# Optimization experiments

Hardware: AMD Instinct MI355X
Metric: run time of the kernel (lower is better)

## Reference

```python
import jax, jax.numpy as jnp
import numpy as np

ALPHA = 0.2  # LeakyReLU negative slope
NEG_INF = -9e15


def _gat_layer(Wh, adj, a, concat):
    """One GraphAttentionLayer given pre-projected Wh [B,N,F].
    Algebraic split of the concat attention: e[b,i,j] = lrelu(Wh[i]@a1 + Wh[j]@a2),
    identical math to matmul(cat(Wh_i, Wh_j), a)."""
    F_ = Wh.shape[-1]
    f1 = Wh @ a[:F_, 0]   # [B,N]
    f2 = Wh @ a[F_:, 0]   # [B,N]
    e = jax.nn.leaky_relu(f1[:, :, None] + f2[:, None, :], negative_slope=ALPHA)  # [B,N,N]
    e = jnp.where(adj > 0, e, NEG_INF)
    att = jax.nn.softmax(e, axis=-1)            # dropout omitted (eval mode)
    h_prime = jnp.einsum('bij,bjf->bif', att, Wh)
    return jax.nn.elu(h_prime) if concat else h_prime


def setup_inputs() -> dict:
    key = jax.random.key(0)
    ks = jax.random.split(key, 9)
    B, N, Fin, H, nH, Fout = 4, 2048, 512, 128, 4, 256
    x = jax.random.normal(ks[0], (B, N, Fin), dtype=jnp.float32)
    adj = jax.random.randint(ks[1], (B, N, N), 0, 2, dtype=jnp.int32)
    mask = jnp.ones((B, N), dtype=jnp.float32)
    s = 0.05
    W_heads = jax.random.normal(ks[2], (nH, Fin, H), dtype=jnp.float32) * s
    a_heads = jax.random.normal(ks[3], (nH, 2 * H, 1), dtype=jnp.float32) * s
    W_out = jax.random.normal(ks[4], (nH * H, Fout), dtype=jnp.float32) * s
    a_out = jax.random.normal(ks[5], (2 * Fout, 1), dtype=jnp.float32) * s
    W_pool = jax.random.normal(ks[6], (Fout, Fout), dtype=jnp.float32) * s
    b_pool = jax.random.normal(ks[7], (Fout,), dtype=jnp.float32) * s
    return {"x": x, "adj": adj, "mask": mask, "W_heads": W_heads, "a_heads": a_heads,
            "W_out": W_out, "a_out": a_out, "W_pool": W_pool, "b_pool": b_pool}


def reference(x, adj, mask, W_heads, a_heads, W_out, a_out, W_pool, b_pool):
    # multi-head GAT layer, heads concatenated (dropout = identity in eval)
    heads = [_gat_layer(x @ W_heads[h], adj, a_heads[h], concat=True)
             for h in range(W_heads.shape[0])]
    xcat = jnp.concatenate(heads, axis=-1)                 # [B,N,nH*H]
    x_out = _gat_layer(xcat @ W_out, adj, a_out, concat=False)  # [B,N,Fout]
    x_out = x_out * mask[:, :, None]
    pooled = x_out.sum(axis=1) / (mask.sum(axis=1, keepdims=True) + 1e-10)
    graph_embedding = jax.nn.relu(pooled @ W_pool + b_pool)
    return graph_embedding, x_out
```

## Files before the change

kernel.cpp:

```cpp
#include <hip/hip_runtime.h>

typedef unsigned short u16;
typedef __attribute__((ext_vector_type(8))) short s8v;
typedef __attribute__((ext_vector_type(8))) unsigned short us8;
typedef __attribute__((ext_vector_type(4))) float f4v;
typedef __attribute__((ext_vector_type(2))) float fp2;

#define L2E 1.4426950408889634f

typedef __attribute__((address_space(1))) void gvoid_t;
typedef __attribute__((address_space(3))) void lvoid_t;

__device__ __forceinline__ u16 f2bf(float f) {
  unsigned u = __builtin_bit_cast(unsigned, f);
  return (u16)((u + 0x7FFFu + ((u >> 16) & 1u)) >> 16);
}
__device__ __forceinline__ float bf2f(u16 h) {
  return __builtin_bit_cast(float, ((unsigned)h) << 16);
}
__device__ __forceinline__ f4v mfma16(s8v a, s8v b, f4v c) {
  return __builtin_amdgcn_mfma_f32_16x16x32_bf16(a, b, c, 0, 0, 0);
}
__device__ __forceinline__ float exp2fast(float x) {
#if __has_builtin(__builtin_amdgcn_exp2f)
  return __builtin_amdgcn_exp2f(x);
#else
  return exp2f(x);
#endif
}
__device__ __forceinline__ void stage16(const u16* g, u16* lds_arr, int slot) {
#if __has_builtin(__builtin_amdgcn_global_load_lds)
  __builtin_amdgcn_global_load_lds((gvoid_t*)(g),
      (lvoid_t*)(lds_arr + (size_t)(slot & ~63) * 8), 16, 0, 0);
#else
  *(us8*)(lds_arr + (size_t)slot * 8) = *(const us8*)g;
#endif
}

__global__ __launch_bounds__(256) void prep_all(const float* __restrict__ x,
                                                u16* __restrict__ xb,
                                                const float* __restrict__ Wh,
                                                u16* __restrict__ Wta,
                                                const float* __restrict__ Wo,
                                                u16* __restrict__ Wto) {
  int bid = blockIdx.x;
  if (bid < 2048) {
    int i = (bid * 256 + threadIdx.x) * 8;
    float4 v0 = *(const float4*)(x + i);
    float4 v1 = *(const float4*)(x + i + 4);
    us8 o;
    o[0] = f2bf(v0.x); o[1] = f2bf(v0.y); o[2] = f2bf(v0.z); o[3] = f2bf(v0.w);
    o[4] = f2bf(v1.x); o[5] = f2bf(v1.y); o[6] = f2bf(v1.z); o[7] = f2bf(v1.w);
    *(us8*)(xb + i) = o;
  } else if (bid < 3072) {
    int idx = (bid - 2048) * 256 + threadIdx.x;
    int h = idx >> 16, k = (idx >> 7) & 511, f = idx & 127;
    Wta[(size_t)(h * 128 + f) * 512 + k] = f2bf(Wh[idx]);
  } else {
    int idx = (bid - 3072) * 256 + threadIdx.x;
    int k = idx >> 8, c = idx & 255;
    Wto[(size_t)c * 512 + k] = f2bf(Wo[idx]);
  }
}

__global__ __launch_bounds__(256) void prep_adj(const int* __restrict__ adj,
                                                unsigned* __restrict__ adjw) {
  int chunk = blockIdx.x * 4 + (threadIdx.x >> 6);
  int l = threadIdx.x & 63;
  int v = adj[(size_t)chunk * 64 + l];
  unsigned long long m = __ballot(v != 0);
  if (l == 0) {
    ((uint2*)adjw)[chunk] = make_uint2((unsigned)m, (unsigned)(m >> 32));
  }
}

__global__ __launch_bounds__(256) void gemm_bf16(const u16* __restrict__ A,
                                                 const u16* __restrict__ Bt,
                                                 u16* __restrict__ Ct, int CO) {
  const int K = 512, N = 2048;
  int m0 = blockIdx.x * 64;
  int n0 = blockIdx.y * 64;
  int t = threadIdx.x;
  int w = t >> 6, l = t & 63, lr = l & 15, lq = l >> 4;
  int wr = w >> 1, wc = w & 1;
  __shared__ u16 As[2][64 * 32];
  __shared__ u16 Bs[2][64 * 32];
  f4v zero4 = {0.f, 0.f, 0.f, 0.f};
  f4v acc[2][2];
#pragma unroll
  for (int i = 0; i < 2; ++i)
#pragma unroll
    for (int j = 0; j < 2; ++j) acc[i][j] = zero4;

  auto stage = [&](int buf, int kt) {
    int k0 = kt * 32;
    int row = t >> 2, ch = t & 3;
    int q = (ch ^ ((row >> 1) & 3)) * 8;
    stage16(A + (size_t)(m0 + row) * K + k0 + q, As[buf], t);
    stage16(Bt + (size_t)(n0 + row) * K + k0 + q, Bs[buf], t);
  };
  stage(0, 0);
  int swz = (lq ^ ((lr >> 1) & 3)) * 8;
  for (int kt = 0; kt < 16; ++kt) {
    __syncthreads();
    if (kt < 15) stage((kt + 1) & 1, kt + 1);
    const u16* as = As[kt & 1];
    const u16* bs = Bs[kt & 1];
    s8v af[2], bfr[2];
#pragma unroll
    for (int rf = 0; rf < 2; ++rf)
      af[rf] = *(const s8v*)&as[(wr * 32 + rf * 16 + lr) * 32 + swz];
#pragma unroll
    for (int nf = 0; nf < 2; ++nf)
      bfr[nf] = *(const s8v*)&bs[(wc * 32 + nf * 16 + lr) * 32 + swz];
#pragma unroll
    for (int rf = 0; rf < 2; ++rf)
#pragma unroll
      for (int nf = 0; nf < 2; ++nf)
        acc[rf][nf] = mfma16(af[rf], bfr[nf], acc[rf][nf]);
  }
  int bidx = m0 >> 11;
  int nr0 = m0 & 2047;
#pragma unroll
  for (int rf = 0; rf < 2; ++rf) {
#pragma unroll
    for (int nf = 0; nf < 2; ++nf) {
      int col = n0 + wc * 32 + nf * 16 + lr;
      int nr = nr0 + wr * 32 + rf * 16 + lq * 4;
      f4v a = acc[rf][nf];
      ushort4 v = make_ushort4(f2bf(a[0]), f2bf(a[1]), f2bf(a[2]), f2bf(a[3]));
      *(ushort4*)&Ct[((size_t)bidx * CO + col) * N + nr] = v;
    }
  }
}

__global__ __launch_bounds__(256) void fkern(const u16* __restrict__ Wht,
                                             const float* __restrict__ a,
                                             float* __restrict__ f1L,
                                             float* __restrict__ f2L, int COLS,
                                             int F) {
  const int N = 2048;
  int h = blockIdx.z, b = blockIdx.y;
  int nl = threadIdx.x & 63, fc = threadIdx.x >> 6;
  int n = blockIdx.x * 64 + nl;
  int F4 = F >> 2;
  const u16* colp = Wht + ((size_t)(b * COLS + h * F + fc * F4)) * N + n;
  const float* ah = a + h * 2 * F + fc * F4;
  float a1 = 0.f, a2 = 0.f;
  for (int c = 0; c < F4; ++c) {
    float v = bf2f(colp[(size_t)c * N]);
    a1 = fmaf(v, ah[c], a1);
    a2 = fmaf(v, ah[F + c], a2);
  }
  __shared__ float r1[4][64], r2[4][64];
  r1[fc][nl] = a1;
  r2[fc][nl] = a2;
  __syncthreads();
  if (fc == 0) {
    float s1 = r1[0][nl] + r1[1][nl] + r1[2][nl] + r1[3][nl];
    float s2 = r2[0][nl] + r2[1][nl] + r2[2][nl] + r2[3][nl];
    f1L[(size_t)(h * 4 + b) * N + n] = s1 * L2E;
    f2L[(size_t)(h * 4 + b) * N + n] = s2 * L2E;
  }
}

__global__ __launch_bounds__(256) void fmax_kern(const float* __restrict__ f2L,
                                                 float* __restrict__ f2m) {
  int row = blockIdx.x;
  const float* p = f2L + (size_t)row * 2048;
  int t = threadIdx.x;
  float v = -__builtin_inff();
  for (int k = 0; k < 8; ++k) v = fmaxf(v, p[t + k * 256]);
#pragma unroll
  for (int d = 1; d < 64; d <<= 1) v = fmaxf(v, __shfl_xor(v, d));
  __shared__ float wm[4];
  if ((t & 63) == 0) wm[t >> 6] = v;
  __syncthreads();
  if (t == 0) f2m[row] = fmaxf(fmaxf(wm[0], wm[1]), fmaxf(wm[2], wm[3]));
}

template <int CT, int WR, bool ELU>
__global__ __launch_bounds__(256, 2) void attn_kernel(
    const u16* __restrict__ Wht, const float* __restrict__ f1L,
    const float* __restrict__ f2L, const float* __restrict__ f2max,
    const unsigned* __restrict__ adjw, const float* __restrict__ mask,
    void* __restrict__ outp, float* __restrict__ pool) {
  const int N = 2048;
  constexpr int WC = 4 / WR;
  constexpr int NF = 8 / WC;
  constexpr int NCH = CT / 128;
  constexpr int ROWS = WR * 16;
  constexpr int NT = 2048 / ROWS;
  constexpr int FHD = (CT == 512) ? 1 : 0;
  int kb = blockIdx.x;
  int x = kb & 7, g = kb >> 3;
  int p = x + 8 * (g / NT);
  int it = g % NT;
  int b = p / NCH, ch = p % NCH;
  int i0 = it * ROWS, col0 = ch * 128;
  int fh = FHD ? ch : 0;
  int t = threadIdx.x;
  int w = t >> 6, l = t & 63, lr = l & 15, lq = l >> 4;
  int wc = w & (WC - 1), wrs = w / WC;

  __shared__ u16 Vs[2][128 * 64];
  __shared__ unsigned adjs[ROWS * 65];
  __shared__ float f2s[2048];

  const float* f1p = f1L + (size_t)(fh * 4 + b) * N + i0;
  const float* f2p = f2L + (size_t)(fh * 4 + b) * N;
  float f2m = f2max[fh * 4 + b];
  float f1v = f1p[wrs * 16 + lr];
  float su = f1v + f2m;
  float M = fmaxf(su, 0.2f * su);
  float c1 = f1v - M;
  float c2 = 0.2f * f1v - M;
  fp2 c1p = {c1, c1}, c2p = {c2, c2}, k2p = {0.2f, 0.2f};
  const u16* vbase = Wht + (size_t)(b * CT + col0) * 2048;

  for (int i = t; i < ROWS * 64; i += 256) {
    int row = i >> 6, wd = i & 63;
    adjs[row * 65 + wd] = adjw[(size_t)(b * N + i0 + row) * 64 + wd];
  }
  for (int i = t; i < 2048; i += 256) f2s[i] = f2p[i];

  auto stage = [&](int buf, int kt) {
    int k0 = kt * 64;
#pragma unroll
    for (int j2 = 0; j2 < 4; ++j2) {
      int s = j2 * 256 + t;
      int c = s >> 3, q = s & 7;
      stage16(vbase + (size_t)c * 2048 + k0 + (q ^ (c & 7)) * 8, Vs[buf], s);
    }
  };
  stage(0, 0);

  f4v zero4 = {0.f, 0.f, 0.f, 0.f};
  f4v acc[NF], accs = zero4;
#pragma unroll
  for (int j = 0; j < NF; ++j) acc[j] = zero4;
  s8v ones;
#pragma unroll
  for (int i = 0; i < 8; ++i) ones[i] = (short)0x3F80;

  for (int kt = 0; kt < 32; ++kt) {
    __syncthreads();
    if (kt < 31) stage((kt + 1) & 1, kt + 1);
    const u16* vs = Vs[kt & 1];
#pragma unroll
    for (int kk = 0; kk < 2; ++kk) {
      int jt = kt * 2 + kk;
      s8v vf[NF];
#pragma unroll
      for (int nf = 0; nf < NF; ++nf) {
        int c = wc * 64 + nf * 16 + lr;
        int chn = (kk * 4 + lq) ^ (lr & 7);
        vf[nf] = *(const s8v*)&vs[c * 64 + chn * 8];
      }
      float4 fa = *(const float4*)&f2s[jt * 32 + lq * 8];
      float4 fb = *(const float4*)&f2s[jt * 32 + lq * 8 + 4];
      float f2c[8] = {fa.x, fa.y, fa.z, fa.w, fb.x, fb.y, fb.z, fb.w};
      unsigned awl = adjs[(wrs * 16 + lr) * 65 + jt] >> (lq * 8);
      union { s8v v; unsigned u[4]; } pk;
#pragma unroll
      for (int ep = 0; ep < 4; ++ep) {
        fp2 fpair = {f2c[2 * ep], f2c[2 * ep + 1]};
        fp2 tA = c1p + fpair;
        fp2 tB = __builtin_elementwise_fma(k2p, fpair, c2p);
        float p0 = exp2fast(fmaxf(tA[0], tB[0]));
        p0 = ((awl >> (2 * ep)) & 1u) ? p0 : 0.f;
        float p1 = exp2fast(fmaxf(tA[1], tB[1]));
        p1 = ((awl >> (2 * ep + 1)) & 1u) ? p1 : 0.f;
        asm("v_cvt_pk_bf16_f32 %0, %1, %2"
            : "=v"(pk.u[ep]) : "v"(p0), "v"(p1));
      }
      s8v pa = pk.v;
      accs = mfma16(pa, ones, accs);
#pragma unroll
      for (int nf = 0; nf < NF; ++nf)
        acc[nf] = mfma16(pa, vf[nf], acc[nf]);
    }
  }
  f4v i4;
#pragma unroll
  for (int r = 0; r < 4; ++r) i4[r] = 1.f / fmaxf(accs[r], 1e-30f);
  int rowb = i0 + wrs * 16 + lq * 4;
  if constexpr (ELU) {
#pragma unroll
    for (int nf = 0; nf < NF; ++nf) {
      int col = col0 + wc * 64 + nf * 16 + lr;
#pragma unroll
      for (int r = 0; r < 4; ++r) {
        float v = acc[nf][r] * i4[r];
        v = v > 0.f ? v : exp2fast(v * L2E) - 1.f;
        ((u16*)outp)[(size_t)(b * N + rowb + r) * CT + col] = f2bf(v);
      }
    }
  } else {
    float mk[4];
#pragma unroll
    for (int r = 0; r < 4; ++r) mk[r] = mask[b * N + rowb + r];
#pragma unroll
    for (int nf = 0; nf < NF; ++nf) {
      int col = col0 + wc * 64 + nf * 16 + lr;
      float cs = 0.f;
#pragma unroll
      for (int r = 0; r < 4; ++r) {
        float vm = acc[nf][r] * i4[r] * mk[r];
        ((float*)outp)[(size_t)(b * N + rowb + r) * CT + col] = vm;
        cs += vm;
      }
      cs += __shfl_xor(cs, 16);
      cs += __shfl_xor(cs, 32);
      if (l < 16) atomicAdd(&pool[b * 256 + col], cs);
    }
  }
}

__global__ __launch_bounds__(256) void pool2(const float* __restrict__ pool,
                                             const float* __restrict__ mask,
                                             const float* __restrict__ Wp,
                                             const float* __restrict__ bp,
                                             float* __restrict__ out) {
  int b = blockIdx.x, f = threadIdx.x;
  __shared__ float pv[256];
  __shared__ float ds[256];
  float m = 0.f;
#pragma unroll
  for (int k = 0; k < 8; ++k) m += mask[b * 2048 + f + k * 256];
  ds[f] = m;
  __syncthreads();
  for (int s = 128; s > 0; s >>= 1) {
    if (f < s) ds[f] += ds[f + s];
    __syncthreads();
  }
  float inv = 1.f / (ds[0] + 1e-10f);
  pv[f] = pool[b * 256 + f] * inv;
  __syncthreads();
  float acc = bp[f];
  for (int c = 0; c < 256; ++c) acc = fmaf(pv[c], Wp[c * 256 + f], acc);
  out[b * 256 + f] = fmaxf(acc, 0.f);
}

extern "C" void kernel_launch(void* const* d_in, const int* in_sizes, int n_in,
                              void* d_out, int out_size, void* d_ws,
                              size_t ws_size, hipStream_t stream) {
  (void)in_sizes; (void)n_in; (void)out_size; (void)ws_size;
  const float* x = (const float*)d_in[0];
  const int* adj = (const int*)d_in[1];
  const float* mask = (const float*)d_in[2];
  const float* Whds = (const float*)d_in[3];
  const float* ahds = (const float*)d_in[4];
  const float* Wout = (const float*)d_in[5];
  const float* aout = (const float*)d_in[6];
  const float* Wpool = (const float*)d_in[7];
  const float* bpool = (const float*)d_in[8];
  float* out = (float*)d_out;

  char* ws = (char*)d_ws;
  size_t off = 0;
  auto take = [&](size_t n) {
    char* p = ws + off;
    off += (n + 255) & ~(size_t)255;
    return p;
  };
  u16* xb = (u16*)take(8192ull * 512 * 2);
  u16* Wta = (u16*)take(512ull * 512 * 2);
  u16* Wto = (u16*)take(256ull * 512 * 2);
  unsigned* adjw = (unsigned*)take(4ull * 2048 * 64 * 4);
  u16* Wht = (u16*)take(4ull * 512 * 2048 * 2);
  float* f1a = (float*)take(4ull * 4 * 2048 * 4);
  float* f2a = (float*)take(4ull * 4 * 2048 * 4);
  u16* xcat = (u16*)take(8192ull * 512 * 2);
  u16* Wh2t = (u16*)take(4ull * 256 * 2048 * 2);
  float* f1b = (float*)take(4ull * 2048 * 4);
  float* f2b = (float*)take(4ull * 2048 * 4);
  float* f2ma = (float*)take(16 * 4);
  float* f2mb = (float*)take(4 * 4);
  float* pool = (float*)take(1024 * 4);

  prep_all<<<3584, 256, 0, stream>>>(x, xb, Whds, Wta, Wout, Wto);
  prep_adj<<<65536, 256, 0, stream>>>(adj, adjw);
  gemm_bf16<<<dim3(128, 8), 256, 0, stream>>>(xb, Wta, Wht, 512);
  fkern<<<dim3(32, 4, 4), 256, 0, stream>>>(Wht, ahds, f1a, f2a, 512, 128);
  fmax_kern<<<16, 256, 0, stream>>>(f2a, f2ma);
  attn_kernel<512, 4, true><<<512, 256, 0, stream>>>(
      Wht, f1a, f2a, f2ma, adjw, nullptr, xcat, nullptr);
  gemm_bf16<<<dim3(128, 4), 256, 0, stream>>>(xcat, Wto, Wh2t, 256);
  fkern<<<dim3(32, 4, 1), 256, 0, stream>>>(Wh2t, aout, f1b, f2b, 256, 256);
  fmax_kern<<<4, 256, 0, stream>>>(f2b, f2mb);
  hipMemsetAsync(pool, 0, 1024 * 4, stream);
  attn_kernel<256, 2, false><<<512, 256, 0, stream>>>(
      Wh2t, f1b, f2b, f2mb, adjw, mask, out + 1024, pool);
  pool2<<<4, 256, 0, stream>>>(pool, mask, Wpool, bpool, out);
}
```

Measured before the change: 167.4 us.

## Add split-K attention kernel for output GAT layer with in-block reduction

Replaces the second-layer attention kernel with a dedicated kernel in which each block handles 16 rows and all 256 output features, and its four waves each cover a quarter of the neighbour dimension (split-K). Partial accumulators and softmax denominators are reduced through shared memory before the mask, normalisation and pooling atomics. Per-wave LDS staging of V tiles is double-issued using explicit waitcnt and sched_barrier. This changes how work is spread across the grid and avoids recomputing attention probabilities per column tile, at the cost of 16 accumulator tiles per wave (register pressure) and extra shared-memory reduction traffic.

```diff
diff --git a/kernel.cpp b/kernel.cpp
--- a/kernel.cpp
+++ b/kernel.cpp
@@ -285,36 +285,149 @@
 #pragma unroll
   for (int r = 0; r < 4; ++r) i4[r] = 1.f / fmaxf(accs[r], 1e-30f);
   int rowb = i0 + wrs * 16 + lq * 4;
-  if constexpr (ELU) {
-#pragma unroll
-    for (int nf = 0; nf < NF; ++nf) {
-      int col = col0 + wc * 64 + nf * 16 + lr;
-#pragma unroll
-      for (int r = 0; r < 4; ++r) {
-        float v = acc[nf][r] * i4[r];
-        v = v > 0.f ? v : exp2fast(v * L2E) - 1.f;
-        ((u16*)outp)[(size_t)(b * N + rowb + r) * CT + col] = f2bf(v);
+#pragma unroll
+  for (int nf = 0; nf < NF; ++nf) {
+    int col = col0 + wc * 64 + nf * 16 + lr;
+#pragma unroll
+    for (int r = 0; r < 4; ++r) {
+      float v = acc[nf][r] * i4[r];
+      v = v > 0.f ? v : exp2fast(v * L2E) - 1.f;
+      ((u16*)outp)[(size_t)(b * N + rowb + r) * CT + col] = f2bf(v);
+    }
+  }
+  (void)mask; (void)pool;
+}
+
+__global__ __launch_bounds__(256, 2) void attn2_kernel(
+    const u16* __restrict__ Wht, const float* __restrict__ f1L,
+    const float* __restrict__ f2L, const float* __restrict__ f2max,
+    const unsigned* __restrict__ adjw, const float* __restrict__ mask,
+    float* __restrict__ outp, float* __restrict__ pool) {
+  const int N = 2048;
+  int kb = blockIdx.x;
+  int b = (kb & 7) >> 1;
+  int it = ((kb >> 3) << 1) | (kb & 1);
+  int i0 = it * 16;
+  int t = threadIdx.x;
+  int w = t >> 6, l = t & 63, lr = l & 15, lq = l >> 4;
+
+  __shared__ __attribute__((aligned(16))) u16 Vs[4][8192];
+  __shared__ unsigned adjs[16 * 65];
+  __shared__ float f2s[2048];
+  __shared__ float sums[4][16];
+
+  const float* f1p = f1L + (size_t)b * N + i0;
+  const float* f2p = f2L + (size_t)b * N;
+  float f2m = f2max[b];
+  float f1v = f1p[lr];
+  float su = f1v + f2m;
+  float M = fmaxf(su, 0.2f * su);
+  float c1 = f1v - M;
+  float c2 = 0.2f * f1v - M;
+  fp2 c1p = {c1, c1}, c2p = {c2, c2}, k2p = {0.2f, 0.2f};
+  const u16* vb = Wht + (size_t)b * 256 * 2048;
+  int j0base = w * 512;
+
+  for (int i = t; i < 16 * 64; i += 256) {
+    int row = i >> 6, wd = i & 63;
+    adjs[row * 65 + wd] = adjw[(size_t)(b * N + i0 + row) * 64 + wd];
+  }
+  for (int i = t; i < 2048; i += 256) f2s[i] = f2p[i];
+  __syncthreads();
+
+  u16* Vsw = Vs[w];
+  auto stage = [&](int kt) {
+    int j0 = j0base + kt * 32;
+#pragma unroll
+    for (int j2 = 0; j2 < 16; ++j2) {
+      int s = j2 * 64 + l;
+      int c = s >> 2, q = s & 3;
+      stage16(vb + (size_t)c * 2048 + j0 + (q ^ (((c >> 3) & 1) << 1)) * 8,
+              Vsw, s);
+    }
+  };
+  stage(0);
+
+  f4v zero4 = {0.f, 0.f, 0.f, 0.f};
+  f4v acc[16], accs = zero4;
+#pragma unroll
+  for (int j = 0; j < 16; ++j) acc[j] = zero4;
+  s8v ones;
+#pragma unroll
+  for (int i = 0; i < 8; ++i) ones[i] = (short)0x3F80;
+  int chunk = (lq ^ (((lr >> 3) & 1) << 1)) * 8;
+
+  for (int kt = 0; kt < 16; ++kt) {
+    int j0 = j0base + kt * 32;
+    float4 fa = *(const float4*)&f2s[j0 + lq * 8];
+    float4 fb = *(const float4*)&f2s[j0 + lq * 8 + 4];
+    float f2c[8] = {fa.x, fa.y, fa.z, fa.w, fb.x, fb.y, fb.z, fb.w};
+    unsigned awl = adjs[lr * 65 + w * 16 + kt] >> (lq * 8);
+    union { s8v v; unsigned u[4]; } pk;
+#pragma unroll
+    for (int ep = 0; ep < 4; ++ep) {
+      fp2 fpair = {f2c[2 * ep], f2c[2 * ep + 1]};
+      fp2 tA = c1p + fpair;
+      fp2 tB = __builtin_elementwise_fma(k2p, fpair, c2p);
+      float p0 = exp2fast(fmaxf(tA[0], tB[0]));
+      p0 = ((awl >> (2 * ep)) & 1u) ? p0 : 0.f;
+      float p1 = exp2fast(fmaxf(tA[1], tB[1]));
+      p1 = ((awl >> (2 * ep + 1)) & 1u) ? p1 : 0.f;
+      asm("v_cvt_pk_bf16_f32 %0, %1, %2"
+          : "=v"(pk.u[ep]) : "v"(p0), "v"(p1));
+    }
+    s8v pa = pk.v;
+    __builtin_amdgcn_s_waitcnt(0x0F70);
+    __builtin_amdgcn_sched_barrier(0);
+#pragma unroll
+    for (int g4 = 0; g4 < 4; ++g4) {
+      s8v vf[4];
+#pragma unroll
+      for (int n4 = 0; n4 < 4; ++n4) {
+        int c = (g4 * 4 + n4) * 16 + lr;
+        vf[n4] = *(const s8v*)&Vsw[c * 32 + chunk];
       }
-    }
-  } else {
-    float mk[4];
-#pragma unroll
-    for (int r = 0; r < 4; ++r) mk[r] = mask[b * N + rowb + r];
-#pragma unroll
-    for (int nf = 0; nf < NF; ++nf) {
-      int col = col0 + wc * 64 + nf * 16 + lr;
-      float cs = 0.f;
-#pragma unroll
-      for (int r = 0; r < 4; ++r) {
-        float vm = acc[nf][r] * i4[r] * mk[r];
-        ((float*)outp)[(size_t)(b * N + rowb + r) * CT + col] = vm;
-        cs += vm;
-      }
-      cs += __shfl_xor(cs, 16);
-      cs += __shfl_xor(cs, 32);
-      if (l < 16) atomicAdd(&pool[b * 256 + col], cs);
-    }
-  }
+#pragma unroll
+      for (int n4 = 0; n4 < 4; ++n4)
+        acc[g4 * 4 + n4] = mfma16(pa, vf[n4], acc[g4 * 4 + n4]);
+    }
+    accs = mfma16(pa, ones, accs);
+    if (kt < 15) {
+      __builtin_amdgcn_s_waitcnt(0xC07F);
+      __builtin_amdgcn_sched_barrier(0);
+      stage(kt + 1);
+    }
+  }
+
+  __syncthreads();
+  float* accm = (float*)&Vs[0][0];
+  if (lr == 0) {
+#pragma unroll
+    for (int r = 0; r < 4; ++r) sums[w][lq * 4 + r] = accs[r];
+  }
+  float* am = accm + w * 16 * 256;
+#pragma unroll
+  for (int nf = 0; nf < 16; ++nf)
+#pragma unroll
+    for (int r = 0; r < 4; ++r)
+      am[(lq * 4 + r) * 256 + nf * 16 + lr] = acc[nf][r];
+  __syncthreads();
+  float invs[16];
+#pragma unroll
+  for (int row = 0; row < 16; ++row) {
+    float s = sums[0][row] + sums[1][row] + sums[2][row] + sums[3][row];
+    invs[row] = 1.f / fmaxf(s, 1e-30f);
+  }
+  float cs = 0.f;
+#pragma unroll
+  for (int row = 0; row < 16; ++row) {
+    float v = accm[row * 256 + t] + accm[4096 + row * 256 + t] +
+              accm[8192 + row * 256 + t] + accm[12288 + row * 256 + t];
+    v *= invs[row] * mask[(size_t)b * N + i0 + row];
+    outp[(size_t)(b * N + i0 + row) * 256 + t] = v;
+    cs += v;
+  }
+  atomicAdd(&pool[b * 256 + t], cs);
 }
 
 __global__ __launch_bounds__(256) void pool2(const float* __restrict__ pool,
@@ -390,7 +503,7 @@
   fkern<<<dim3(32, 4, 1), 256, 0, stream>>>(Wh2t, aout, f1b, f2b, 256, 256);
   fmax_kern<<<4, 256, 0, stream>>>(f2b, f2mb);
   hipMemsetAsync(pool, 0, 1024 * 4, stream);
-  attn_kernel<256, 2, false><<<512, 256, 0, stream>>>(
-      Wh2t, f1b, f2b, f2mb, adjw, mask, out + 1024, pool);
+  attn2_kernel<<<512, 256, 0, stream>>>(Wh2t, f1b, f2b, f2mb, adjw, mask,
+                                        out + 1024, pool);
   pool2<<<4, 256, 0, stream>>>(pool, mask, Wpool, bpool, out);
 }
```

After: 177.4 us. 1.06x slower.
